# Performance work log

Measured on AMD Instinct MI355X. Metric: run time of the kernel, lower is better.

The kernel has to match this reference:

```python
import jax, jax.numpy as jnp
import numpy as np

D = 256       # in_channels == hd_channels
H = 8         # heads
HC = D // H   # head dim = 32
NV = 30000    # variables
NC = 60000    # clauses
E = 120000    # edges per polarity


def setup_inputs() -> dict:
    key = jax.random.key(0)
    ks = jax.random.split(key, 16)
    std = 0.02
    v = jax.random.normal(ks[0], (NV, D), jnp.float32)
    c = jax.random.normal(ks[1], (NC, D), jnp.float32)
    # adj row0 indexes clauses (c), row1 indexes variables (v)
    adj_pos = jnp.stack([jax.random.randint(ks[2], (E,), 0, NC),
                         jax.random.randint(ks[3], (E,), 0, NV)]).astype(jnp.int32)
    adj_neg = jnp.stack([jax.random.randint(ks[4], (E,), 0, NC),
                         jax.random.randint(ks[5], (E,), 0, NV)]).astype(jnp.int32)
    # shared projections (ModuleList([lin]*2) shares one module)
    Wq = jax.random.normal(ks[6], (D, D), jnp.float32) * std
    bq = jnp.zeros((D,), jnp.float32)
    Wkv = jax.random.normal(ks[7], (D, 2 * D), jnp.float32) * std
    bkv = jnp.zeros((2 * D,), jnp.float32)
    ffn_v_w1 = jax.random.normal(ks[8], (D, D), jnp.float32) * std
    ffn_v_b1 = jnp.zeros((D,), jnp.float32)
    ffn_v_w2 = jax.random.normal(ks[9], (D, D), jnp.float32) * std
    ffn_v_b2 = jnp.zeros((D,), jnp.float32)
    ffn_c_w1 = jax.random.normal(ks[10], (D, D), jnp.float32) * std
    ffn_c_b1 = jnp.zeros((D,), jnp.float32)
    ffn_c_w2 = jax.random.normal(ks[11], (D, D), jnp.float32) * std
    ffn_c_b2 = jnp.zeros((D,), jnp.float32)
    ones = jnp.ones((D,), jnp.float32)
    zeros = jnp.zeros((D,), jnp.float32)
    return dict(v=v, c=c, adj_pos=adj_pos, adj_neg=adj_neg,
                Wq=Wq, bq=bq, Wkv=Wkv, bkv=bkv,
                ffn_v_w1=ffn_v_w1, ffn_v_b1=ffn_v_b1, ffn_v_w2=ffn_v_w2, ffn_v_b2=ffn_v_b2,
                ffn_c_w1=ffn_c_w1, ffn_c_b1=ffn_c_b1, ffn_c_w2=ffn_c_w2, ffn_c_b2=ffn_c_b2,
                ln_att_v_g=ones, ln_att_v_b=zeros, ln_ffn_v_g=ones, ln_ffn_v_b=zeros,
                ln_att_c_g=ones, ln_att_c_b=zeros, ln_ffn_c_g=ones, ln_ffn_c_b=zeros)


def _split(x):
    return x.reshape(x.shape[0], H, HC)


def _ln(x, g, b, eps=1e-5):
    m = jnp.mean(x, axis=-1, keepdims=True)
    va = jnp.mean(jnp.square(x - m), axis=-1, keepdims=True)
    return (x - m) * jax.lax.rsqrt(va + eps) * g + b


def _seg_softmax(x, seg, n):
    m = jax.ops.segment_max(x, seg, num_segments=n)      # (n, H)
    e = jnp.exp(x - m[seg])
    s = jax.ops.segment_sum(e, seg, num_segments=n)
    return e / s[seg]


def _sparse_attn(q, k, val, e_q, e_k, n_q):
    # q: (Lq,H,HC); k,val: (Lk,H,HC); per-edge dot -> segment softmax -> scatter aggregate
    qk = jnp.einsum('ehc,ehc->eh', q[e_q], k[e_k]) * (1.0 / np.sqrt(HC))
    alpha = _seg_softmax(qk, e_q, n_q)                   # (E,H)
    return jax.ops.segment_sum(alpha[:, :, None] * val[e_k], e_q, num_segments=n_q)


def _cross(x, y, adj, Wq, bq, Wkv, bkv):
    # adj[0] indexes y, adj[1] indexes x
    ey, ex = adj[0], adj[1]
    qx = _split(x @ Wq + bq)
    ky, vy = jnp.split(y @ Wkv + bkv, 2, axis=-1)
    w = _sparse_attn(qx, _split(ky), _split(vy), ex, ey, x.shape[0])   # x queries, transposed edges
    qy = _split(y @ Wq + bq)
    kx, vx = jnp.split(x @ Wkv + bkv, 2, axis=-1)
    u = _sparse_attn(qy, _split(kx), _split(vx), ey, ex, y.shape[0])   # y queries
    return w.reshape(x.shape[0], D), u.reshape(y.shape[0], D)


def _ffn(x, w1, b1, w2, b2):
    return jax.nn.gelu(x @ w1 + b1, approximate=False) @ w2 + b2


def reference(v, c, adj_pos, adj_neg, Wq, bq, Wkv, bkv,
              ffn_v_w1, ffn_v_b1, ffn_v_w2, ffn_v_b2,
              ffn_c_w1, ffn_c_b1, ffn_c_w2, ffn_c_b2,
              ln_att_v_g, ln_att_v_b, ln_ffn_v_g, ln_ffn_v_b,
              ln_att_c_g, ln_att_c_b, ln_ffn_c_g, ln_ffn_c_b):
    wp, up = _cross(v, c, adj_pos, Wq, bq, Wkv, bkv)
    wn, un = _cross(v, c, adj_neg, Wq, bq, Wkv, bkv)
    v1 = _ln(v + (wp + wn), ln_att_v_g, ln_att_v_b)
    c1 = _ln(c + (up + un), ln_att_c_g, ln_att_c_b)
    v2 = _ln(v1 + _ffn(v1, ffn_v_w1, ffn_v_b1, ffn_v_w2, ffn_v_b2), ln_ffn_v_g, ln_ffn_v_b)
    c2 = _ln(c1 + _ffn(c1, ffn_c_w1, ffn_c_b1, ffn_c_w2, ffn_c_b2), ln_ffn_c_g, ln_ffn_c_b)
    return (v2, c2)
```

## Files before the change

kernel.cpp:

```cpp
#include <hip/hip_runtime.h>
#include <math.h>

#define DD 256
#define NH 8

typedef __attribute__((ext_vector_type(8))) short short8;
typedef __attribute__((ext_vector_type(4))) float floatx4;

__device__ __forceinline__ float b2f(unsigned short u) {
    return __uint_as_float(((unsigned)u) << 16);
}
__device__ __forceinline__ unsigned short f2b(float f) {
    unsigned u = __float_as_uint(f);
    return (unsigned short)((u + 0x7fffu + ((u >> 16) & 1u)) >> 16);
}

__global__ void detect_dtype(const unsigned* __restrict__ ones_words, int* __restrict__ flag) {
    flag[0] = (ones_words[0] == 0x3F800000u) ? 0 : 1;
}

__device__ __forceinline__ void load8(const void* base, size_t off, int f32, unsigned short* dst) {
    if (f32) {
        const float4* p = (const float4*)((const float*)base + off);
        float4 x = p[0], y = p[1];
        dst[0] = f2b(x.x); dst[1] = f2b(x.y); dst[2] = f2b(x.z); dst[3] = f2b(x.w);
        dst[4] = f2b(y.x); dst[5] = f2b(y.y); dst[6] = f2b(y.z); dst[7] = f2b(y.w);
    } else {
        *(uint4*)dst = *(const uint4*)((const unsigned short*)base + off);
    }
}

__global__ void wt_build(const void* __restrict__ Wq, const void* __restrict__ Wkv,
                         const void* __restrict__ f1v, const void* __restrict__ f1c,
                         const void* __restrict__ f2v, const void* __restrict__ f2c,
                         short* __restrict__ wt, const int* __restrict__ flagp)
{
    const int extf = (*flagp == 0);
    const void* src; int N; size_t dst0;
    switch (blockIdx.z) {
        case 0:  src = Wq;  N = 256; dst0 = 0;          break;
        case 1:  src = Wkv; N = 512; dst0 = 256 * 256;  break;
        case 2:  src = f1v; N = 256; dst0 = 768 * 256;  break;
        case 3:  src = f1c; N = 256; dst0 = 1024 * 256; break;
        case 4:  src = f2v; N = 256; dst0 = 1280 * 256; break;
        default: src = f2c; N = 256; dst0 = 1536 * 256; break;
    }
    int n0 = blockIdx.x * 32, k0 = blockIdx.y * 32;
    if (n0 >= N) return;
    __shared__ short tile[32][33];
    int tx = threadIdx.x & 31, ty = threadIdx.x >> 5;
    #pragma unroll
    for (int i = 0; i < 32; i += 8) {
        int k = k0 + ty + i, n = n0 + tx;
        float val = extf ? ((const float*)src)[(size_t)k * N + n]
                         : b2f(((const unsigned short*)src)[(size_t)k * N + n]);
        tile[ty + i][tx] = (short)f2b(val);
    }
    __syncthreads();
    #pragma unroll
    for (int i = 0; i < 32; i += 8)
        wt[dst0 + (size_t)(n0 + ty + i) * 256 + k0 + tx] = tile[tx][ty + i];
}

__launch_bounds__(256)
__global__ void proj_gemm(const void* __restrict__ va, const void* __restrict__ ca,
                          int NVr, int NCr, int bv,
                          const short* __restrict__ wt,
                          const void* __restrict__ bq, const void* __restrict__ bkv,
                          unsigned short* __restrict__ qbuf, unsigned short* __restrict__ kvbuf,
                          const int* __restrict__ flagp)
{
    const int extf = (*flagp == 0);
    __shared__ __align__(16) short As[64][264];
    __shared__ __align__(16) short Bs[64][32];
    const int t = threadIdx.x;
    const int wave = t >> 6, lane = t & 63;
    const int bx = blockIdx.x;
    int grow0, nrows; const void* asrc; size_t abase;
    if (bx < bv) { grow0 = bx * 64; asrc = va; abase = (size_t)grow0 * DD; nrows = NVr - grow0; }
    else { int mc0 = (bx - bv) * 64; grow0 = NVr + mc0; asrc = ca; abase = (size_t)mc0 * DD; nrows = NCr - mc0; }
    if (nrows > 64) nrows = 64;
    {
        const int r = t >> 2, cb = (t & 3) * 8;
        #pragma unroll
        for (int cc = 0; cc < 8; ++cc) {
            int col = cb + cc * 32;
            unsigned short a8[8] = {0, 0, 0, 0, 0, 0, 0, 0};
            if (r < nrows) load8(asrc, abase + (size_t)r * DD + col, extf, a8);
            *(uint4*)(&As[r][col]) = *(const uint4*)a8;
        }
    }
    __syncthreads();
    const int fr = lane & 15, fq = lane >> 4;
    const int brow = t >> 2, bcol = (t & 3) * 8;
    for (int nc = 0; nc < 12; ++nc) {
        const short* wtc = wt + (size_t)nc * 64 * 256;
        floatx4 acc[4] = {};
        for (int k0 = 0; k0 < 256; k0 += 32) {
            *(uint4*)(&Bs[brow][bcol]) = *(const uint4*)(wtc + (size_t)brow * 256 + k0 + bcol);
            __syncthreads();
            short8 af = *(const short8*)(&As[wave * 16 + fr][k0 + fq * 8]);
            #pragma unroll
            for (int j = 0; j < 4; ++j) {
                short8 bf = *(const short8*)(&Bs[j * 16 + fr][fq * 8]);
                acc[j] = __builtin_amdgcn_mfma_f32_16x16x32_bf16(af, bf, acc[j], 0, 0, 0);
            }
            __syncthreads();
        }
        unsigned short* outp; int ldo, colbase; const void* bias;
        if (nc < 4) { outp = qbuf;  ldo = 256; colbase = nc * 64;       bias = bq;  }
        else        { outp = kvbuf; ldo = 512; colbase = (nc - 4) * 64; bias = bkv; }
        #pragma unroll
        for (int j = 0; j < 4; ++j) {
            int col = colbase + j * 16 + fr;
            float bvv = extf ? ((const float*)bias)[col] : b2f(((const unsigned short*)bias)[col]);
            #pragma unroll
            for (int r = 0; r < 4; ++r) {
                int rr = wave * 16 + fq * 4 + r;
                if (rr < nrows)
                    outp[(size_t)(grow0 + rr) * ldo + col] = f2b(acc[j][r] + bvv);
            }
        }
    }
}

template<int EPI>
__launch_bounds__(256)
__global__ void ffn_gemm(const unsigned short* __restrict__ A,
                         int NVr, int NCr, int bv,
                         const short* __restrict__ wtV, const short* __restrict__ wtC,
                         const void* __restrict__ biasV, const void* __restrict__ biasC,
                         void* __restrict__ outp, const int* __restrict__ flagp)
{
    const int extf = (*flagp == 0);
    __shared__ __align__(16) short As[64][264];
    __shared__ __align__(16) short Bs[64][32];
    const int t = threadIdx.x;
    const int wave = t >> 6, lane = t & 63;
    const int bx = blockIdx.x;
    int grow0, nrows; const short* wtp; const void* bias;
    if (bx < bv) { grow0 = bx * 64; nrows = NVr - grow0; wtp = wtV; bias = biasV; }
    else { grow0 = NVr + (bx - bv) * 64; nrows = NVr + NCr - grow0; wtp = wtC; bias = biasC; }
    if (nrows > 64) nrows = 64;
    {
        const int r = t >> 2, cb = (t & 3) * 8;
        #pragma unroll
        for (int cc = 0; cc < 8; ++cc) {
            int col = cb + cc * 32;
            uint4 a8 = make_uint4(0u, 0u, 0u, 0u);
            if (r < nrows) a8 = *(const uint4*)(A + (size_t)(grow0 + r) * DD + col);
            *(uint4*)(&As[r][col]) = a8;
        }
    }
    __syncthreads();
    const int fr = lane & 15, fq = lane >> 4;
    const int brow = t >> 2, bcol = (t & 3) * 8;
    for (int nc = 0; nc < 4; ++nc) {
        const short* wtc = wtp + (size_t)nc * 64 * 256;
        floatx4 acc[4] = {};
        for (int k0 = 0; k0 < 256; k0 += 32) {
            *(uint4*)(&Bs[brow][bcol]) = *(const uint4*)(wtc + (size_t)brow * 256 + k0 + bcol);
            __syncthreads();
            short8 af = *(const short8*)(&As[wave * 16 + fr][k0 + fq * 8]);
            #pragma unroll
            for (int j = 0; j < 4; ++j) {
                short8 bf = *(const short8*)(&Bs[j * 16 + fr][fq * 8]);
                acc[j] = __builtin_amdgcn_mfma_f32_16x16x32_bf16(af, bf, acc[j], 0, 0, 0);
            }
            __syncthreads();
        }
        #pragma unroll
        for (int j = 0; j < 4; ++j) {
            int col = nc * 64 + j * 16 + fr;
            float bvv = extf ? ((const float*)bias)[col] : b2f(((const unsigned short*)bias)[col]);
            #pragma unroll
            for (int r = 0; r < 4; ++r) {
                int rr = wave * 16 + fq * 4 + r;
                if (rr < nrows) {
                    float x = acc[j][r] + bvv;
                    if (EPI == 1) {
                        x = 0.5f * x * (1.0f + erff(x * 0.70710678118654752f));
                        ((unsigned short*)outp)[(size_t)(grow0 + rr) * DD + col] = f2b(x);
                    } else {
                        ((float*)outp)[(size_t)(grow0 + rr) * DD + col] = x;
                    }
                }
            }
        }
    }
}

__global__ void csr_count(const int* __restrict__ ap, const int* __restrict__ an,
                          int E, int NV, int NT, int* __restrict__ counts) {
    int e = blockIdx.x * 256 + threadIdx.x;
    if (e >= E) return;
    atomicAdd(&counts[ap[E + e]], 1);
    atomicAdd(&counts[NV + ap[e]], 1);
    atomicAdd(&counts[NT + an[E + e]], 1);
    atomicAdd(&counts[NT + NV + an[e]], 1);
}

__global__ void scan_block(const int* __restrict__ counts, int* __restrict__ offs,
                           int* __restrict__ bsum, int n) {
    __shared__ int sm[256];
    int i = blockIdx.x * 256 + threadIdx.x;
    int x = (i < n) ? counts[i] : 0;
    sm[threadIdx.x] = x;
    __syncthreads();
    #pragma unroll
    for (int d = 1; d < 256; d <<= 1) {
        int t = (threadIdx.x >= d) ? sm[threadIdx.x - d] : 0;
        __syncthreads();
        sm[threadIdx.x] += t;
        __syncthreads();
    }
    if (i < n) offs[i] = sm[threadIdx.x] - x;
    if (threadIdx.x == 255) bsum[blockIdx.x] = sm[255];
}

__global__ void scan_bsum(int* __restrict__ bsum, int nb) {
    __shared__ int sm[256];
    __shared__ int carry;
    if (threadIdx.x == 0) carry = 0;
    __syncthreads();
    for (int base = 0; base < nb; base += 256) {
        int i = base + threadIdx.x;
        int x = (i < nb) ? bsum[i] : 0;
        sm[threadIdx.x] = x;
        __syncthreads();
        #pragma unroll
        for (int d = 1; d < 256; d <<= 1) {
            int t = (threadIdx.x >= d) ? sm[threadIdx.x - d] : 0;
            __syncthreads();
            sm[threadIdx.x] += t;
            __syncthreads();
        }
        int excl = sm[threadIdx.x] - x + carry;
        if (i < nb) bsum[i] = excl;
        __syncthreads();
        if (threadIdx.x == 0) carry += sm[255];
        __syncthreads();
    }
}

__global__ void scan_add(int* __restrict__ offs, const int* __restrict__ bsum, int n) {
    int i = blockIdx.x * 256 + threadIdx.x;
    if (i < n) offs[i] += bsum[blockIdx.x];
}

__global__ void csr_fill(const int* __restrict__ ap, const int* __restrict__ an,
                         int E, int NV, int NT, int* __restrict__ offs, int* __restrict__ eids) {
    int e = blockIdx.x * 256 + threadIdx.x;
    if (e >= E) return;
    int p;
    p = atomicAdd(&offs[ap[E + e]], 1);            eids[p] = e * 2;
    p = atomicAdd(&offs[NV + ap[e]], 1);           eids[p] = e * 2 + 1;
    p = atomicAdd(&offs[NT + an[E + e]], 1);       eids[p] = e * 2;
    p = atomicAdd(&offs[NT + NV + an[e]], 1);      eids[p] = e * 2 + 1;
}

__launch_bounds__(256)
__global__ void edge_logits(const int* __restrict__ adj, int E, int NV,
                            const unsigned short* __restrict__ qbuf,
                            const unsigned short* __restrict__ kvbuf,
                            float* __restrict__ qk)
{
    int t = blockIdx.x * 256 + threadIdx.x;
    if (t >= E * 16) return;
    int e = t >> 4, rem = t & 15;
    int dir = rem >> 3, h = rem & 7;
    int ce = adj[e], xe = adj[E + e];
    int qrow = dir ? (NV + ce) : xe;
    int krow = dir ? xe : (NV + ce);
    const unsigned short* qp = qbuf + (size_t)qrow * DD + h * 32;
    const unsigned short* kp = kvbuf + (size_t)krow * 512 + h * 32;
    float s = 0.f;
    #pragma unroll
    for (int i = 0; i < 4; ++i) {
        uint4 qv = ((const uint4*)qp)[i];
        uint4 kv = ((const uint4*)kp)[i];
        const unsigned short* qa = (const unsigned short*)&qv;
        const unsigned short* ka = (const unsigned short*)&kv;
        #pragma unroll
        for (int j = 0; j < 8; ++j) s += b2f(qa[j]) * b2f(ka[j]);
    }
    qk[t] = s * 0.17677669529663689f;
}

__launch_bounds__(256)
__global__ void seg_attn(const int* __restrict__ offs_end, const int* __restrict__ counts,
                         const int* __restrict__ eids, const int* __restrict__ adj,
                         int E, int NV, const float* __restrict__ qk,
                         const unsigned short* __restrict__ kvbuf,
                         float* __restrict__ osum, int NT, int acc_mode)
{
    int seg = blockIdx.x * 4 + (threadIdx.x >> 6);
    if (seg >= NT) return;
    int lane = threadIdx.x & 63;
    int deg = counts[seg];
    float4* op = (float4*)(osum + (size_t)seg * DD) + lane;
    if (deg == 0) {
        if (!acc_mode) *op = make_float4(0.f, 0.f, 0.f, 0.f);
        return;
    }
    int beg = offs_end[seg] - deg;
    int slot = lane >> 3, h = lane & 7;
    float m = -1e30f;
    for (int j = slot; j < deg; j += 8)
        m = fmaxf(m, qk[(size_t)eids[beg + j] * 8 + h]);
    m = fmaxf(m, __shfl_xor(m, 8));
    m = fmaxf(m, __shfl_xor(m, 16));
    m = fmaxf(m, __shfl_xor(m, 32));
    float s = 0.f;
    for (int j = slot; j < deg; j += 8)
        s += __expf(qk[(size_t)eids[beg + j] * 8 + h] - m);
    s += __shfl_xor(s, 8);
    s += __shfl_xor(s, 16);
    s += __shfl_xor(s, 32);
    int h3 = lane >> 3;
    float m3 = __shfl(m, h3);
    float rs3 = 1.f / __shfl(s, h3);
    float a0 = 0.f, a1 = 0.f, a2 = 0.f, a3 = 0.f;
    for (int j = 0; j < deg; ++j) {
        int eid = eids[beg + j];
        int e = eid >> 1, dir = eid & 1;
        int krow = dir ? adj[E + e] : (NV + adj[e]);
        float alpha = __expf(qk[(size_t)eid * 8 + h3] - m3) * rs3;
        ushort4 vv = *(const ushort4*)(kvbuf + (size_t)krow * 512 + DD + lane * 4);
        a0 += alpha * b2f(vv.x);
        a1 += alpha * b2f(vv.y);
        a2 += alpha * b2f(vv.z);
        a3 += alpha * b2f(vv.w);
    }
    float4 o;
    if (acc_mode) {
        float4 old = *op;
        o.x = old.x + a0; o.y = old.y + a1; o.z = old.z + a2; o.w = old.w + a3;
    } else {
        o.x = a0; o.y = a1; o.z = a2; o.w = a3;
    }
    *op = o;
}

template<int BASE_EXT, int OUT_EXT>
__launch_bounds__(256)
__global__ void ln_res(const void* __restrict__ baseA, const void* __restrict__ baseB,
                       const float* __restrict__ add,
                       const void* __restrict__ gA, const void* __restrict__ bA,
                       const void* __restrict__ gB, const void* __restrict__ bB,
                       void* __restrict__ out, int NA, int Ntot, const int* __restrict__ flagp)
{
    int row = blockIdx.x * 4 + (threadIdx.x >> 6);
    if (row >= Ntot) return;
    int lane = threadIdx.x & 63;
    const int extf = (*flagp == 0);
    const void *base, *g, *b;
    size_t roff;
    if (row < NA) { base = baseA; g = gA; b = bA; roff = (size_t)row * DD; }
    else          { base = baseB; g = gB; b = bB; roff = (size_t)(row - NA) * DD; }
    float4 a = ((const float4*)(add + (size_t)row * DD))[lane];
    float y0, y1, y2, y3;
    if (BASE_EXT && extf) {
        float4 t = ((const float4*)((const float*)base + roff))[lane];
        y0 = t.x; y1 = t.y; y2 = t.z; y3 = t.w;
    } else {
        ushort4 t = ((const ushort4*)((const unsigned short*)base + roff))[lane];
        y0 = b2f(t.x); y1 = b2f(t.y); y2 = b2f(t.z); y3 = b2f(t.w);
    }
    y0 += a.x; y1 += a.y; y2 += a.z; y3 += a.w;
    float s = y0 + y1 + y2 + y3;
    #pragma unroll
    for (int off = 32; off; off >>= 1) s += __shfl_xor(s, off);
    float mean = s * (1.0f / DD);
    float d0 = y0 - mean, d1 = y1 - mean, d2 = y2 - mean, d3 = y3 - mean;
    float v = d0 * d0 + d1 * d1 + d2 * d2 + d3 * d3;
    #pragma unroll
    for (int off = 32; off; off >>= 1) v += __shfl_xor(v, off);
    float rstd = rsqrtf(v * (1.0f / DD) + 1e-5f);
    float g0, g1, g2, g3, t0, t1, t2, t3;
    if (extf) {
        float4 gg = ((const float4*)g)[lane]; float4 bt = ((const float4*)b)[lane];
        g0 = gg.x; g1 = gg.y; g2 = gg.z; g3 = gg.w;
        t0 = bt.x; t1 = bt.y; t2 = bt.z; t3 = bt.w;
    } else {
        ushort4 gg = ((const ushort4*)g)[lane]; ushort4 bt = ((const ushort4*)b)[lane];
        g0 = b2f(gg.x); g1 = b2f(gg.y); g2 = b2f(gg.z); g3 = b2f(gg.w);
        t0 = b2f(bt.x); t1 = b2f(bt.y); t2 = b2f(bt.z); t3 = b2f(bt.w);
    }
    float o0 = d0 * rstd * g0 + t0, o1 = d1 * rstd * g1 + t1;
    float o2 = d2 * rstd * g2 + t2, o3 = d3 * rstd * g3 + t3;
    if (OUT_EXT && extf) {
        float4 o; o.x = o0; o.y = o1; o.z = o2; o.w = o3;
        ((float4*)((float*)out + (size_t)row * DD))[lane] = o;
    } else {
        ushort4 o;
        o.x = f2b(o0); o.y = f2b(o1); o.z = f2b(o2); o.w = f2b(o3);
        ((ushort4*)((unsigned short*)out + (size_t)row * DD))[lane] = o;
    }
}

extern "C" void kernel_launch(void* const* d_in, const int* in_sizes, int n_in,
                              void* d_out, int out_size, void* d_ws, size_t ws_size,
                              hipStream_t stream)
{
    const void* v   = d_in[0];
    const void* c   = d_in[1];
    const int* adj_pos = (const int*)d_in[2];
    const int* adj_neg = (const int*)d_in[3];
    const void* Wq  = d_in[4];
    const void* bq  = d_in[5];
    const void* Wkv = d_in[6];
    const void* bkv = d_in[7];
    const void* fvw1 = d_in[8];
    const void* fvb1 = d_in[9];
    const void* fvw2 = d_in[10];
    const void* fvb2 = d_in[11];
    const void* fcw1 = d_in[12];
    const void* fcb1 = d_in[13];
    const void* fcw2 = d_in[14];
    const void* fcb2 = d_in[15];
    const void* lavg = d_in[16];
    const void* lavb = d_in[17];
    const void* lfvg = d_in[18];
    const void* lfvb = d_in[19];
    const void* lacg = d_in[20];
    const void* lacb = d_in[21];
    const void* lfcg = d_in[22];
    const void* lfcb = d_in[23];

    const int NV = in_sizes[0] / DD;
    const int NC = in_sizes[1] / DD;
    const int NT = NV + NC;
    const int E  = in_sizes[2] / 2;

    char* w = (char*)d_ws;
    int* flagp = (int*)w;
    size_t off = 256;
    float* osum = (float*)(w + off);
    off += (size_t)NT * DD * 4;
    unsigned short* qbuf = (unsigned short*)(w + off);
    off += (size_t)NT * DD * 2;
    unsigned short* kvbuf = (unsigned short*)(w + off);
    off += (size_t)NT * DD * 4;
    float* qkbuf = (float*)(w + off);
    off += (size_t)E * 16 * 4;
    int* counts = (int*)(w + off);
    off += (size_t)2 * NT * 4;
    int* offs = (int*)(w + off);
    off += (size_t)2 * NT * 4;
    int* eids = (int*)(w + off);
    off += (size_t)4 * E * 4;
    int* bsum = (int*)(w + off);
    off += 4096;
    short* wt = (short*)(w + off);

    dim3 blk(256);
    const int bv = (NV + 63) / 64, bc = (NC + 63) / 64;
    const int nbE = (E + 255) / 256;
    const int n2 = 2 * NT, nb2 = (n2 + 255) / 256;

    detect_dtype<<<dim3(1), dim3(1), 0, stream>>>((const unsigned*)lavg, flagp);
    wt_build<<<dim3(16, 8, 6), blk, 0, stream>>>(Wq, Wkv, fvw1, fcw1, fvw2, fcw2, wt, flagp);

    proj_gemm<<<dim3(bv + bc), blk, 0, stream>>>(v, c, NV, NC, bv, wt, bq, bkv, qbuf, kvbuf, flagp);

    hipMemsetAsync(counts, 0, (size_t)n2 * 4, stream);
    csr_count<<<dim3(nbE), blk, 0, stream>>>(adj_pos, adj_neg, E, NV, NT, counts);
    scan_block<<<dim3(nb2), blk, 0, stream>>>(counts, offs, bsum, n2);
    scan_bsum<<<dim3(1), blk, 0, stream>>>(bsum, nb2);
    scan_add<<<dim3(nb2), blk, 0, stream>>>(offs, bsum, n2);
    csr_fill<<<dim3(nbE), blk, 0, stream>>>(adj_pos, adj_neg, E, NV, NT, offs, eids);

    for (int p = 0; p < 2; ++p) {
        const int* adj = p ? adj_neg : adj_pos;
        edge_logits<<<dim3((E * 16 + 255) / 256), blk, 0, stream>>>(adj, E, NV, qbuf, kvbuf, qkbuf);
        seg_attn<<<dim3((NT + 3) / 4), blk, 0, stream>>>(offs + (size_t)p * NT, counts + (size_t)p * NT,
                                                         eids, adj, E, NV, qkbuf, kvbuf, osum, NT, p);
    }

    unsigned short* x1 = qbuf;
    ln_res<1, 0><<<dim3((NT + 3) / 4), blk, 0, stream>>>(v, c, osum, lavg, lavb, lacg, lacb,
                                                         x1, NV, NT, flagp);

    unsigned short* hbuf = kvbuf;
    ffn_gemm<1><<<dim3(bv + bc), blk, 0, stream>>>(x1, NV, NC, bv,
                                                   wt + (size_t)768 * 256, wt + (size_t)1024 * 256,
                                                   fvb1, fcb1, hbuf, flagp);
    ffn_gemm<2><<<dim3(bv + bc), blk, 0, stream>>>(hbuf, NV, NC, bv,
                                                   wt + (size_t)1280 * 256, wt + (size_t)1536 * 256,
                                                   fvb2, fcb2, osum, flagp);

    ln_res<0, 1><<<dim3((NT + 3) / 4), blk, 0, stream>>>(x1, x1 + (size_t)NV * DD, osum,
                                                         lfvg, lfvb, lfcg, lfcb,
                                                         d_out, NV, NT, flagp);
}
```

Measured before the change: 787.8 us.

## Keep GEMM A-fragments in registers and read weights directly, dropping LDS staging

The projection and FFN GEMMs now tile 128 rows per block, with each wave owning 32 rows. Each wave loads its A operand fragments straight from global memory into registers once, then streams weight fragments from global/L2 with no shared-memory staging and no __syncthreads. This removes the per-k-step barriers and LDS traffic, and reuses each B fragment across two 16-row MFMA tiles. In exchange it raises register pressure (launch bounds set to 2 blocks) and makes every wave fetch weights from cache independently.

```diff
diff --git a/kernel.cpp b/kernel.cpp
--- a/kernel.cpp
+++ b/kernel.cpp
@@ -62,50 +62,54 @@
         wt[dst0 + (size_t)(n0 + ty + i) * 256 + k0 + tx] = tile[tx][ty + i];
 }
 
-__launch_bounds__(256)
-__global__ void proj_gemm(const void* __restrict__ va, const void* __restrict__ ca,
-                          int NVr, int NCr, int bv,
-                          const short* __restrict__ wt,
-                          const void* __restrict__ bq, const void* __restrict__ bkv,
-                          unsigned short* __restrict__ qbuf, unsigned short* __restrict__ kvbuf,
-                          const int* __restrict__ flagp)
+__launch_bounds__(256, 2)
+__global__ void proj_gemm2(const void* __restrict__ va, const void* __restrict__ ca,
+                           int NVr, int NCr, int bv,
+                           const short* __restrict__ wt,
+                           const void* __restrict__ bq, const void* __restrict__ bkv,
+                           unsigned short* __restrict__ qbuf, unsigned short* __restrict__ kvbuf,
+                           const int* __restrict__ flagp)
 {
     const int extf = (*flagp == 0);
-    __shared__ __align__(16) short As[64][264];
-    __shared__ __align__(16) short Bs[64][32];
     const int t = threadIdx.x;
     const int wave = t >> 6, lane = t & 63;
+    const int fr = lane & 15, fq = lane >> 4;
     const int bx = blockIdx.x;
-    int grow0, nrows; const void* asrc; size_t abase;
-    if (bx < bv) { grow0 = bx * 64; asrc = va; abase = (size_t)grow0 * DD; nrows = NVr - grow0; }
-    else { int mc0 = (bx - bv) * 64; grow0 = NVr + mc0; asrc = ca; abase = (size_t)mc0 * DD; nrows = NCr - mc0; }
-    if (nrows > 64) nrows = 64;
-    {
-        const int r = t >> 2, cb = (t & 3) * 8;
-        #pragma unroll
-        for (int cc = 0; cc < 8; ++cc) {
-            int col = cb + cc * 32;
-            unsigned short a8[8] = {0, 0, 0, 0, 0, 0, 0, 0};
-            if (r < nrows) load8(asrc, abase + (size_t)r * DD + col, extf, a8);
-            *(uint4*)(&As[r][col]) = *(const uint4*)a8;
+    int grow0, nrows, abase_row; const void* asrc;
+    if (bx < bv) { grow0 = bx * 128; asrc = va; abase_row = grow0; nrows = NVr - grow0; }
+    else { int mc0 = (bx - bv) * 128; grow0 = NVr + mc0; asrc = ca; abase_row = mc0; nrows = NCr - mc0; }
+    if (nrows > 128) nrows = 128;
+    const int wrow0 = wave * 32;
+    if (wrow0 >= nrows) return;
+
+    short8 af[2][8];
+    #pragma unroll
+    for (int m = 0; m < 2; ++m) {
+        int r = wrow0 + m * 16 + fr;
+        if (r >= nrows) r = nrows - 1;
+        size_t rowoff = (size_t)(abase_row + r) * DD;
+        #pragma unroll
+        for (int k8 = 0; k8 < 8; ++k8) {
+            __align__(16) unsigned short tmp[8];
+            load8(asrc, rowoff + k8 * 32 + fq * 8, extf, tmp);
+            af[m][k8] = *(const short8*)tmp;
         }
     }
-    __syncthreads();
-    const int fr = lane & 15, fq = lane >> 4;
-    const int brow = t >> 2, bcol = (t & 3) * 8;
+
     for (int nc = 0; nc < 12; ++nc) {
         const short* wtc = wt + (size_t)nc * 64 * 256;
-        floatx4 acc[4] = {};
-        for (int k0 = 0; k0 < 256; k0 += 32) {
-            *(uint4*)(&Bs[brow][bcol]) = *(const uint4*)(wtc + (size_t)brow * 256 + k0 + bcol);
-            __syncthreads();
-            short8 af = *(const short8*)(&As[wave * 16 + fr][k0 + fq * 8]);
+        floatx4 acc[2][4] = {};
+        #pragma unroll
+        for (int k8 = 0; k8 < 8; ++k8) {
+            short8 bf[4];
+            #pragma unroll
+            for (int j = 0; j < 4; ++j)
+                bf[j] = *(const short8*)(wtc + (size_t)(j * 16 + fr) * 256 + k8 * 32 + fq * 8);
             #pragma unroll
             for (int j = 0; j < 4; ++j) {
-                short8 bf = *(const short8*)(&Bs[j * 16 + fr][fq * 8]);
-                acc[j] = __builtin_amdgcn_mfma_f32_16x16x32_bf16(af, bf, acc[j], 0, 0, 0);
+                acc[0][j] = __builtin_amdgcn_mfma_f32_16x16x32_bf16(af[0][k8], bf[j], acc[0][j], 0, 0, 0);
+                acc[1][j] = __builtin_amdgcn_mfma_f32_16x16x32_bf16(af[1][k8], bf[j], acc[1][j], 0, 0, 0);
             }
-            __syncthreads();
         }
         unsigned short* outp; int ldo, colbase; const void* bias;
         if (nc < 4) { outp = qbuf;  ldo = 256; colbase = nc * 64;       bias = bq;  }
@@ -115,74 +119,81 @@
             int col = colbase + j * 16 + fr;
             float bvv = extf ? ((const float*)bias)[col] : b2f(((const unsigned short*)bias)[col]);
             #pragma unroll
-            for (int r = 0; r < 4; ++r) {
-                int rr = wave * 16 + fq * 4 + r;
-                if (rr < nrows)
-                    outp[(size_t)(grow0 + rr) * ldo + col] = f2b(acc[j][r] + bvv);
+            for (int m = 0; m < 2; ++m) {
+                #pragma unroll
+                for (int r = 0; r < 4; ++r) {
+                    int rr = wrow0 + m * 16 + fq * 4 + r;
+                    if (rr < nrows)
+                        outp[(size_t)(grow0 + rr) * ldo + col] = f2b(acc[m][j][r] + bvv);
+                }
             }
         }
     }
 }
 
 template<int EPI>
-__launch_bounds__(256)
-__global__ void ffn_gemm(const unsigned short* __restrict__ A,
-                         int NVr, int NCr, int bv,
-                         const short* __restrict__ wtV, const short* __restrict__ wtC,
-                         const void* __restrict__ biasV, const void* __restrict__ biasC,
-                         void* __restrict__ outp, const int* __restrict__ flagp)
+__launch_bounds__(256, 2)
+__global__ void ffn_gemm2(const unsigned short* __restrict__ A,
+                          int NVr, int NCr, int bv,
+                          const short* __restrict__ wtV, const short* __restrict__ wtC,
+                          const void* __restrict__ biasV, const void* __restrict__ biasC,
+                          void* __restrict__ outp, const int* __restrict__ flagp)
 {
     const int extf = (*flagp == 0);
-    __shared__ __align__(16) short As[64][264];
-    __shared__ __align__(16) short Bs[64][32];
     const int t = threadIdx.x;
     const int wave = t >> 6, lane = t & 63;
+    const int fr = lane & 15, fq = lane >> 4;
     const int bx = blockIdx.x;
     int grow0, nrows; const short* wtp; const void* bias;
-    if (bx < bv) { grow0 = bx * 64; nrows = NVr - grow0; wtp = wtV; bias = biasV; }
-    else { grow0 = NVr + (bx - bv) * 64; nrows = NVr + NCr - grow0; wtp = wtC; bias = biasC; }
-    if (nrows > 64) nrows = 64;
-    {
-        const int r = t >> 2, cb = (t & 3) * 8;
-        #pragma unroll
-        for (int cc = 0; cc < 8; ++cc) {
-            int col = cb + cc * 32;
-            uint4 a8 = make_uint4(0u, 0u, 0u, 0u);
-            if (r < nrows) a8 = *(const uint4*)(A + (size_t)(grow0 + r) * DD + col);
-            *(uint4*)(&As[r][col]) = a8;
-        }
-    }
-    __syncthreads();
-    const int fr = lane & 15, fq = lane >> 4;
-    const int brow = t >> 2, bcol = (t & 3) * 8;
+    if (bx < bv) { grow0 = bx * 128; nrows = NVr - grow0; wtp = wtV; bias = biasV; }
+    else { grow0 = NVr + (bx - bv) * 128; nrows = NVr + NCr - grow0; wtp = wtC; bias = biasC; }
+    if (nrows > 128) nrows = 128;
+    const int wrow0 = wave * 32;
+    if (wrow0 >= nrows) return;
+
+    short8 af[2][8];
+    #pragma unroll
+    for (int m = 0; m < 2; ++m) {
+        int r = wrow0 + m * 16 + fr;
+        if (r >= nrows) r = nrows - 1;
+        const unsigned short* rp = A + (size_t)(grow0 + r) * DD;
+        #pragma unroll
+        for (int k8 = 0; k8 < 8; ++k8)
+            af[m][k8] = *(const short8*)(rp + k8 * 32 + fq * 8);
+    }
+
     for (int nc = 0; nc < 4; ++nc) {
         const short* wtc = wtp + (size_t)nc * 64 * 256;
-        floatx4 acc[4] = {};
-        for (int k0 = 0; k0 < 256; k0 += 32) {
-            *(uint4*)(&Bs[brow][bcol]) = *(const uint4*)(wtc + (size_t)brow * 256 + k0 + bcol);
-            __syncthreads();
-            short8 af = *(const short8*)(&As[wave * 16 + fr][k0 + fq * 8]);
+        floatx4 acc[2][4] = {};
+        #pragma unroll
+        for (int k8 = 0; k8 < 8; ++k8) {
+            short8 bf[4];
+            #pragma unroll
+            for (int j = 0; j < 4; ++j)
+                bf[j] = *(const short8*)(wtc + (size_t)(j * 16 + fr) * 256 + k8 * 32 + fq * 8);
             #pragma unroll
             for (int j = 0; j < 4; ++j) {
-                short8 bf = *(const short8*)(&Bs[j * 16 + fr][fq * 8]);
-                acc[j] = __builtin_amdgcn_mfma_f32_16x16x32_bf16(af, bf, acc[j], 0, 0, 0);
+                acc[0][j] = __builtin_amdgcn_mfma_f32_16x16x32_bf16(af[0][k8], bf[j], acc[0][j], 0, 0, 0);
+                acc[1][j] = __builtin_amdgcn_mfma_f32_16x16x32_bf16(af[1][k8], bf[j], acc[1][j], 0, 0, 0);
             }
-            __syncthreads();
         }
         #pragma unroll
         for (int j = 0; j < 4; ++j) {
             int col = nc * 64 + j * 16 + fr;
             float bvv = extf ? ((const float*)bias)[col] : b2f(((const unsigned short*)bias)[col]);
             #pragma unroll
-            for (int r = 0; r < 4; ++r) {
-                int rr = wave * 16 + fq * 4 + r;
-                if (rr < nrows) {
-                    float x = acc[j][r] + bvv;
-                    if (EPI == 1) {
-                        x = 0.5f * x * (1.0f + erff(x * 0.70710678118654752f));
-                        ((unsigned short*)outp)[(size_t)(grow0 + rr) * DD + col] = f2b(x);
-                    } else {
-                        ((float*)outp)[(size_t)(grow0 + rr) * DD + col] = x;
+            for (int m = 0; m < 2; ++m) {
+                #pragma unroll
+                for (int r = 0; r < 4; ++r) {
+                    int rr = wrow0 + m * 16 + fq * 4 + r;
+                    if (rr < nrows) {
+                        float x = acc[m][j][r] + bvv;
+                        if (EPI == 1) {
+                            x = 0.5f * x * (1.0f + erff(x * 0.70710678118654752f));
+                            ((unsigned short*)outp)[(size_t)(grow0 + rr) * DD + col] = f2b(x);
+                        } else {
+                            ((float*)outp)[(size_t)(grow0 + rr) * DD + col] = x;
+                        }
                     }
                 }
             }
@@ -455,14 +466,15 @@
     short* wt = (short*)(w + off);
 
     dim3 blk(256);
-    const int bv = (NV + 63) / 64, bc = (NC + 63) / 64;
+    const int bv128 = (NV + 127) / 128, bc128 = (NC + 127) / 128;
     const int nbE = (E + 255) / 256;
     const int n2 = 2 * NT, nb2 = (n2 + 255) / 256;
 
     detect_dtype<<<dim3(1), dim3(1), 0, stream>>>((const unsigned*)lavg, flagp);
     wt_build<<<dim3(16, 8, 6), blk, 0, stream>>>(Wq, Wkv, fvw1, fcw1, fvw2, fcw2, wt, flagp);
 
-    proj_gemm<<<dim3(bv + bc), blk, 0, stream>>>(v, c, NV, NC, bv, wt, bq, bkv, qbuf, kvbuf, flagp);
+    proj_gemm2<<<dim3(bv128 + bc128), blk, 0, stream>>>(v, c, NV, NC, bv128, wt, bq, bkv,
+                                                        qbuf, kvbuf, flagp);
 
     hipMemsetAsync(counts, 0, (size_t)n2 * 4, stream);
     csr_count<<<dim3(nbE), blk, 0, stream>>>(adj_pos, adj_neg, E, NV, NT, counts);
@@ -483,12 +495,12 @@
                                                          x1, NV, NT, flagp);
 
     unsigned short* hbuf = kvbuf;
-    ffn_gemm<1><<<dim3(bv + bc), blk, 0, stream>>>(x1, NV, NC, bv,
-                                                   wt + (size_t)768 * 256, wt + (size_t)1024 * 256,
-                                                   fvb1, fcb1, hbuf, flagp);
-    ffn_gemm<2><<<dim3(bv + bc), blk, 0, stream>>>(hbuf, NV, NC, bv,
-                                                   wt + (size_t)1280 * 256, wt + (size_t)1536 * 256,
-                                                   fvb2, fcb2, osum, flagp);
+    ffn_gemm2<1><<<dim3(bv128 + bc128), blk, 0, stream>>>(x1, NV, NC, bv128,
+                                                          wt + (size_t)768 * 256, wt + (size_t)1024 * 256,
+                                                          fvb1, fcb1, hbuf, flagp);
+    ffn_gemm2<2><<<dim3(bv128 + bc128), blk, 0, stream>>>(hbuf, NV, NC, bv128,
+                                                          wt + (size_t)1280 * 256, wt + (size_t)1536 * 256,
+                                                          fvb2, fcb2, osum, flagp);
 
     ln_res<0, 1><<<dim3((NT + 3) / 4), blk, 0, stream>>>(x1, x1 + (size_t)NV * DD, osum,
                                                          lfvg, lfvb, lfcg, lfcb,
```

Result: slower. 854.3 us (+8.4%).

## Double-buffer full-K weight chunks via direct global-to-LDS loads in GEMMs

Applied to the files above, without the earlier changes.

The projection and FFN GEMMs now use 512-thread blocks covering 128 rows. Each 64-column weight chunk is staged whole (all of K) into LDS with global_load_lds and an XOR swizzle, and the next chunk is double-buffered while the current one is computed. This removes the per-K-step syncthreads and the small B tile reloads of the old kernel. The cost is much more LDS per block (about 130 KB), which limits occupancy to one block per CU, and relies on correct swizzle and async-load ordering.

```diff
diff --git a/kernel.cpp b/kernel.cpp
--- a/kernel.cpp
+++ b/kernel.cpp
@@ -13,6 +13,12 @@
 __device__ __forceinline__ unsigned short f2b(float f) {
     unsigned u = __float_as_uint(f);
     return (unsigned short)((u + 0x7fffu + ((u >> 16) & 1u)) >> 16);
+}
+
+__device__ __forceinline__ void gload_lds16(const void* g, void* l) {
+    __builtin_amdgcn_global_load_lds(
+        (const __attribute__((address_space(1))) void*)g,
+        (__attribute__((address_space(3))) void*)l, 16, 0, 0);
 }
 
 __global__ void detect_dtype(const unsigned* __restrict__ ones_words, int* __restrict__ flag) {
@@ -62,50 +68,70 @@
         wt[dst0 + (size_t)(n0 + ty + i) * 256 + k0 + tx] = tile[tx][ty + i];
 }
 
-__launch_bounds__(256)
-__global__ void proj_gemm(const void* __restrict__ va, const void* __restrict__ ca,
-                          int NVr, int NCr, int bv,
-                          const short* __restrict__ wt,
-                          const void* __restrict__ bq, const void* __restrict__ bkv,
-                          unsigned short* __restrict__ qbuf, unsigned short* __restrict__ kvbuf,
-                          const int* __restrict__ flagp)
-{
+
+__device__ __forceinline__ void stage_bchunk(const char* src32k, char* dst, int wave, int lane) {
+    #pragma unroll
+    for (int i = 0; i < 4; ++i) {
+        int So = ((wave * 4 + i) << 10) + lane * 16;
+        int Ls = So ^ (((So >> 9) & 7) << 4);
+        gload_lds16(src32k + Ls, dst + ((wave * 4 + i) << 10));
+    }
+}
+
+__device__ __forceinline__ short8 read_bfrag(const char* bbuf, int row, int bytecol) {
+    int S = (row << 9) + bytecol;
+    S ^= (row & 7) << 4;
+    return *(const short8*)(bbuf + S);
+}
+
+__launch_bounds__(512)
+__global__ void proj_gemm4(const void* __restrict__ va, const void* __restrict__ ca,
+                           int NVr, int NCr, int bv,
+                           const short* __restrict__ wt,
+                           const void* __restrict__ bq, const void* __restrict__ bkv,
+                           unsigned short* __restrict__ qbuf, unsigned short* __restrict__ kvbuf,
+                           const int* __restrict__ flagp)
+{
+    __shared__ __align__(16) short As[128][264];
+    __shared__ __align__(16) char Bs[2][64 * 512];
     const int extf = (*flagp == 0);
-    __shared__ __align__(16) short As[64][264];
-    __shared__ __align__(16) short Bs[64][32];
     const int t = threadIdx.x;
     const int wave = t >> 6, lane = t & 63;
+    const int fr = lane & 15, fq = lane >> 4;
     const int bx = blockIdx.x;
-    int grow0, nrows; const void* asrc; size_t abase;
-    if (bx < bv) { grow0 = bx * 64; asrc = va; abase = (size_t)grow0 * DD; nrows = NVr - grow0; }
-    else { int mc0 = (bx - bv) * 64; grow0 = NVr + mc0; asrc = ca; abase = (size_t)mc0 * DD; nrows = NCr - mc0; }
-    if (nrows > 64) nrows = 64;
+    int grow0, nrows, abase_row; const void* asrc;
+    if (bx < bv) { grow0 = bx * 128; asrc = va; abase_row = grow0; nrows = NVr - grow0; }
+    else { int mc0 = (bx - bv) * 128; grow0 = NVr + mc0; asrc = ca; abase_row = mc0; nrows = NCr - mc0; }
+    if (nrows > 128) nrows = 128;
+
+    stage_bchunk((const char*)wt, Bs[0], wave, lane);
     {
         const int r = t >> 2, cb = (t & 3) * 8;
         #pragma unroll
         for (int cc = 0; cc < 8; ++cc) {
             int col = cb + cc * 32;
-            unsigned short a8[8] = {0, 0, 0, 0, 0, 0, 0, 0};
-            if (r < nrows) load8(asrc, abase + (size_t)r * DD + col, extf, a8);
+            __align__(16) unsigned short a8[8] = {0, 0, 0, 0, 0, 0, 0, 0};
+            if (r < nrows) load8(asrc, (size_t)(abase_row + r) * DD + col, extf, a8);
             *(uint4*)(&As[r][col]) = *(const uint4*)a8;
         }
     }
     __syncthreads();
-    const int fr = lane & 15, fq = lane >> 4;
-    const int brow = t >> 2, bcol = (t & 3) * 8;
+
+    int cur = 0;
     for (int nc = 0; nc < 12; ++nc) {
-        const short* wtc = wt + (size_t)nc * 64 * 256;
+        if (nc + 1 < 12)
+            stage_bchunk((const char*)(wt + (size_t)(nc + 1) * 64 * 256), Bs[cur ^ 1], wave, lane);
         floatx4 acc[4] = {};
-        for (int k0 = 0; k0 < 256; k0 += 32) {
-            *(uint4*)(&Bs[brow][bcol]) = *(const uint4*)(wtc + (size_t)brow * 256 + k0 + bcol);
-            __syncthreads();
-            short8 af = *(const short8*)(&As[wave * 16 + fr][k0 + fq * 8]);
+        #pragma unroll
+        for (int k8 = 0; k8 < 8; ++k8) {
+            short8 af = *(const short8*)(&As[wave * 16 + fr][k8 * 32 + fq * 8]);
+            short8 bf[4];
             #pragma unroll
-            for (int j = 0; j < 4; ++j) {
-                short8 bf = *(const short8*)(&Bs[j * 16 + fr][fq * 8]);
-                acc[j] = __builtin_amdgcn_mfma_f32_16x16x32_bf16(af, bf, acc[j], 0, 0, 0);
-            }
-            __syncthreads();
+            for (int j = 0; j < 4; ++j)
+                bf[j] = read_bfrag(Bs[cur], j * 16 + fr, k8 * 64 + fq * 16);
+            #pragma unroll
+            for (int j = 0; j < 4; ++j)
+                acc[j] = __builtin_amdgcn_mfma_f32_16x16x32_bf16(af, bf[j], acc[j], 0, 0, 0);
         }
         unsigned short* outp; int ldo, colbase; const void* bias;
         if (nc < 4) { outp = qbuf;  ldo = 256; colbase = nc * 64;       bias = bq;  }
@@ -121,27 +147,32 @@
                     outp[(size_t)(grow0 + rr) * ldo + col] = f2b(acc[j][r] + bvv);
             }
         }
+        __syncthreads();
+        cur ^= 1;
     }
 }
 
 template<int EPI>
-__launch_bounds__(256)
-__global__ void ffn_gemm(const unsigned short* __restrict__ A,
-                         int NVr, int NCr, int bv,
-                         const short* __restrict__ wtV, const short* __restrict__ wtC,
-                         const void* __restrict__ biasV, const void* __restrict__ biasC,
-                         void* __restrict__ outp, const int* __restrict__ flagp)
-{
+__launch_bounds__(512)
+__global__ void ffn_gemm4(const unsigned short* __restrict__ A,
+                          int NVr, int NCr, int bv,
+                          const short* __restrict__ wtV, const short* __restrict__ wtC,
+                          const void* __restrict__ biasV, const void* __restrict__ biasC,
+                          void* __restrict__ outp, const int* __restrict__ flagp)
+{
+    __shared__ __align__(16) short As[128][264];
+    __shared__ __align__(16) char Bs[2][64 * 512];
     const int extf = (*flagp == 0);
-    __shared__ __align__(16) short As[64][264];
-    __shared__ __align__(16) short Bs[64][32];
     const int t = threadIdx.x;
     const int wave = t >> 6, lane = t & 63;
+    const int fr = lane & 15, fq = lane >> 4;
     const int bx = blockIdx.x;
     int grow0, nrows; const short* wtp; const void* bias;
-    if (bx < bv) { grow0 = bx * 64; nrows = NVr - grow0; wtp = wtV; bias = biasV; }
-    else { grow0 = NVr + (bx - bv) * 64; nrows = NVr + NCr - grow0; wtp = wtC; bias = biasC; }
-    if (nrows > 64) nrows = 64;
+    if (bx < bv) { grow0 = bx * 128; nrows = NVr - grow0; wtp = wtV; bias = biasV; }
+    else { grow0 = NVr + (bx - bv) * 128; nrows = NVr + NCr - grow0; wtp = wtC; bias = biasC; }
+    if (nrows > 128) nrows = 128;
+
+    stage_bchunk((const char*)wtp, Bs[0], wave, lane);
     {
         const int r = t >> 2, cb = (t & 3) * 8;
         #pragma unroll
@@ -153,21 +184,22 @@
         }
     }
     __syncthreads();
-    const int fr = lane & 15, fq = lane >> 4;
-    const int brow = t >> 2, bcol = (t & 3) * 8;
+
+    int cur = 0;
     for (int nc = 0; nc < 4; ++nc) {
-        const short* wtc = wtp + (size_t)nc * 64 * 256;
+        if (nc + 1 < 4)
+            stage_bchunk((const char*)(wtp + (size_t)(nc + 1) * 64 * 256), Bs[cur ^ 1], wave, lane);
         floatx4 acc[4] = {};
-        for (int k0 = 0; k0 < 256; k0 += 32) {
-            *(uint4*)(&Bs[brow][bcol]) = *(const uint4*)(wtc + (size_t)brow * 256 + k0 + bcol);
-            __syncthreads();
-            short8 af = *(const short8*)(&As[wave * 16 + fr][k0 + fq * 8]);
+        #pragma unroll
+        for (int k8 = 0; k8 < 8; ++k8) {
+            short8 af = *(const short8*)(&As[wave * 16 + fr][k8 * 32 + fq * 8]);
+            short8 bf[4];
             #pragma unroll
-            for (int j = 0; j < 4; ++j) {
-                short8 bf = *(const short8*)(&Bs[j * 16 + fr][fq * 8]);
-                acc[j] = __builtin_amdgcn_mfma_f32_16x16x32_bf16(af, bf, acc[j], 0, 0, 0);
-            }
-            __syncthreads();
+            for (int j = 0; j < 4; ++j)
+                bf[j] = read_bfrag(Bs[cur], j * 16 + fr, k8 * 64 + fq * 16);
+            #pragma unroll
+            for (int j = 0; j < 4; ++j)
+                acc[j] = __builtin_amdgcn_mfma_f32_16x16x32_bf16(af, bf[j], acc[j], 0, 0, 0);
         }
         #pragma unroll
         for (int j = 0; j < 4; ++j) {
@@ -187,6 +219,8 @@
                 }
             }
         }
+        __syncthreads();
+        cur ^= 1;
     }
 }
 
@@ -454,15 +488,16 @@
     off += 4096;
     short* wt = (short*)(w + off);
 
-    dim3 blk(256);
-    const int bv = (NV + 63) / 64, bc = (NC + 63) / 64;
+    dim3 blk(256), blk512(512);
+    const int bv = (NV + 127) / 128, bc = (NC + 127) / 128;
     const int nbE = (E + 255) / 256;
     const int n2 = 2 * NT, nb2 = (n2 + 255) / 256;
 
     detect_dtype<<<dim3(1), dim3(1), 0, stream>>>((const unsigned*)lavg, flagp);
     wt_build<<<dim3(16, 8, 6), blk, 0, stream>>>(Wq, Wkv, fvw1, fcw1, fvw2, fcw2, wt, flagp);
 
-    proj_gemm<<<dim3(bv + bc), blk, 0, stream>>>(v, c, NV, NC, bv, wt, bq, bkv, qbuf, kvbuf, flagp);
+    proj_gemm4<<<dim3(bv + bc), blk512, 0, stream>>>(v, c, NV, NC, bv, wt, bq, bkv,
+                                                     qbuf, kvbuf, flagp);
 
     hipMemsetAsync(counts, 0, (size_t)n2 * 4, stream);
     csr_count<<<dim3(nbE), blk, 0, stream>>>(adj_pos, adj_neg, E, NV, NT, counts);
@@ -483,12 +518,12 @@
                                                          x1, NV, NT, flagp);
 
     unsigned short* hbuf = kvbuf;
-    ffn_gemm<1><<<dim3(bv + bc), blk, 0, stream>>>(x1, NV, NC, bv,
-                                                   wt + (size_t)768 * 256, wt + (size_t)1024 * 256,
-                                                   fvb1, fcb1, hbuf, flagp);
-    ffn_gemm<2><<<dim3(bv + bc), blk, 0, stream>>>(hbuf, NV, NC, bv,
-                                                   wt + (size_t)1280 * 256, wt + (size_t)1536 * 256,
-                                                   fvb2, fcb2, osum, flagp);
+    ffn_gemm4<1><<<dim3(bv + bc), blk512, 0, stream>>>(x1, NV, NC, bv,
+                                                       wt + (size_t)768 * 256, wt + (size_t)1024 * 256,
+                                                       fvb1, fcb1, hbuf, flagp);
+    ffn_gemm4<2><<<dim3(bv + bc), blk512, 0, stream>>>(hbuf, NV, NC, bv,
+                                                       wt + (size_t)1280 * 256, wt + (size_t)1536 * 256,
+                                                       fvb2, fcb2, osum, flagp);
 
     ln_res<0, 1><<<dim3((NT + 3) / 4), blk, 0, stream>>>(x1, x1 + (size_t)NV * DD, osum,
                                                          lfvg, lfvb, lfcg, lfcb,
```

Result: no change. 803.0 us (+1.9%).
